# Performance work log

Measured on AMD Instinct MI355X. Metric: run time of the kernel, lower is better.

## Reference

```python
import jax, jax.numpy as jnp
import numpy as np

B, CIN, COUT, H, W, KK = 1, 32, 64, 181, 360, 4
NNZ_PER, NNZ_PER1 = 9, 4


def _make_psi(rng, K, H, W, nnz_per):
    # Sparse DISCO basis in COO form for longitude 0 (shift-invariant in lon).
    E = K * H * nnz_per
    seg = np.repeat(np.arange(K * H, dtype=np.int32), nnz_per)  # k*H + ho
    ho = seg % H
    dlat = rng.integers(-1, 2, size=E).astype(np.int32)
    hi = np.clip(ho + dlat, 0, H - 1).astype(np.int32)
    wi = (rng.integers(-1, 2, size=E).astype(np.int32)) % W
    vals = (rng.normal(size=E) * 0.2).astype(np.float32)
    return seg, hi, wi, vals


def setup_inputs() -> dict:
    rng = np.random.default_rng(0)
    key = jax.random.key(0)
    ks = jax.random.split(key, 5)
    x = jax.random.normal(ks[0], (B, CIN, H, W), dtype=jnp.float32)
    # spherical quadrature weights: sin(colatitude) * cell area
    theta = np.linspace(0.0, np.pi, H)
    qw = (np.sin(theta) * (np.pi / (H - 1)) * (2.0 * np.pi / W)).astype(np.float32)
    qw = np.maximum(qw, 1e-8).reshape(H, 1)
    seg, hi, wi, vals = _make_psi(rng, KK, H, W, NNZ_PER)
    seg1, hi1, wi1, vals1 = _make_psi(rng, 1, H, W, NNZ_PER1)
    w_depth = jax.random.normal(ks[1], (CIN, KK), dtype=jnp.float32) / np.sqrt(KK)
    w_point = jax.random.normal(ks[2], (COUT, CIN), dtype=jnp.float32) / np.sqrt(CIN)
    bias = jax.random.normal(ks[3], (COUT,), dtype=jnp.float32) * 0.02
    return {
        "x": x,
        "quad_w": jnp.asarray(qw),
        "vals": jnp.asarray(vals),
        "seg": jnp.asarray(seg),
        "hi": jnp.asarray(hi),
        "wi": jnp.asarray(wi),
        "w_depth": w_depth,
        "vals1": jnp.asarray(vals1),
        "seg1": jnp.asarray(seg1),
        "hi1": jnp.asarray(hi1),
        "wi1": jnp.asarray(wi1),
        "w_point": w_point,
        "bias": bias,
        "K": KK,
    }


def _disco_contract(x, vals, seg, hi, wi, K):
    # x: [B,C,H,W]; COO psi at lon 0; out[b,c,k,ho,wo] =
    #   sum_{e: seg[e]==k*H+ho} vals[e] * x[b,c,hi[e],(wi[e]+wo) mod W]
    Bq, C, Hq, Wq = x.shape
    rows = x[:, :, hi, :]                                        # [B,C,E,W]
    col = (wi[:, None] + jnp.arange(Wq, dtype=wi.dtype)[None, :]) % Wq  # [E,W]
    rolled = jnp.take_along_axis(rows, col[None, None, :, :], axis=3)   # [B,C,E,W]
    weighted = rolled * vals[None, None, :, None]
    out = jax.ops.segment_sum(weighted.transpose(2, 0, 1, 3), seg,
                              num_segments=K * Hq)               # [K*H,B,C,W]
    return out.reshape(K, Hq, Bq, C, Wq).transpose(2, 3, 0, 1, 4)  # [B,C,K,H,W]


def reference(x, quad_w, vals, seg, hi, wi, w_depth, vals1, seg1, hi1, wi1,
              w_point, bias, K):
    # depthwise DISCO conv (groups=C_in, no bias)
    xq = x * quad_w                                   # quadrature weighting
    xd = _disco_contract(xq, vals, seg, hi, wi, K)    # [B,C,K,H,W]
    y = jnp.einsum("ck,bckhw->bchw", w_depth, xd)     # per-channel K mix
    # pointwise DISCO conv (kernel_shape=1) = CLinear
    yq = y * quad_w
    z = _disco_contract(yq, vals1, seg1, hi1, wi1, 1)[:, :, 0]  # [B,C,H,W]
    out = jnp.einsum("oc,bchw->bohw", w_point, z) + bias[None, :, None, None]
    return out
```

## Files before the change

kernel.cpp:

```cpp
#include <hip/hip_runtime.h>


#define H_    181
#define W_    360
#define CIN_  32
#define COUT_ 64
#define K_    4
#define NNZ_  9
#define NNZ1_ 4
#define HW_   (H_*W_)
#define NT_   (NNZ1_*K_*NNZ_)

__global__ __launch_bounds__(512) void sepconv_one(
    const float* __restrict__ x, const float* __restrict__ quad_w,
    const float* __restrict__ vals, const int* __restrict__ hi,
    const int* __restrict__ wi, const float* __restrict__ w_depth,
    const float* __restrict__ vals1, const int* __restrict__ hi1,
    const int* __restrict__ wi1, const float* __restrict__ w_point,
    const float* __restrict__ bias, float* __restrict__ out)
{
    const int bx = blockIdx.x;
    const int h  = (bx & 7) * 23 + (bx >> 3);
    if (h >= H_) return;
    const int seg = blockIdx.y;
    const int w0  = seg * 64;
    const int pxn = (seg == 5) ? 40 : 64;
    const int gn  = pxn >> 2;
    const int tid = threadIdx.x;

    __shared__ float Tval[NT_];
    __shared__ int   Tbin[NT_];
    __shared__ float S[K_][25];
    __shared__ float C[CIN_][25];
    __shared__ float zs[64][33];

    const int g = tid & 15;
    const int c = tid >> 4;
    const bool act = (g < gn);

    int rowoff[5];
    #pragma unroll
    for (int rb = 0; rb < 5; ++rb) {
        int r = h - 2 + rb;
        r = (r < 0) ? 0 : ((r > H_ - 1) ? H_ - 1 : r);
        rowoff[rb] = r * W_;
    }

    const int bw = w0 + g * 4;
    const int cA = (bw + W_ - 4) % W_;
    const int cB = bw;
    const int cC = (bw + 4) % W_;

    float4 L[15];
    if (act) {
        const float* xc = x + c * HW_;
        #pragma unroll
        for (int rb = 0; rb < 5; ++rb) {
            const float* xr = xc + rowoff[rb];
            L[rb * 3 + 0] = *(const float4*)(xr + cA);
            L[rb * 3 + 1] = *(const float4*)(xr + cB);
            L[rb * 3 + 2] = *(const float4*)(xr + cC);
        }
    }

    if (tid < NT_) {
        const int a   = tid / 36;
        const int rem = tid - a * 36;
        const int k   = rem / 9;
        const int j   = rem - k * 9;
        const int e1  = h * NNZ1_ + a;
        const int m   = hi1[e1];
        const int w1  = wi1[e1];
        const int d1  = (w1 == 1) ? 1 : ((w1 == 0) ? 0 : -1);
        const int e   = (k * H_ + m) * NNZ_ + j;
        const int r   = hi[e];
        const int ww  = wi[e];
        const int d   = (ww == 1) ? 1 : ((ww == 0) ? 0 : -1);
        Tval[tid] = vals1[e1] * quad_w[m] * vals[e] * quad_w[r];
        Tbin[tid] = (r - h + 2) * 5 + (d1 + d + 2);
    }
    __syncthreads();

    if (tid < K_ * 25) {
        const int k   = tid / 25;
        const int bin = tid - k * 25;
        float s = 0.f;
        #pragma unroll
        for (int a = 0; a < NNZ1_; ++a)
            #pragma unroll
            for (int j = 0; j < NNZ_; ++j) {
                const int t2 = a * 36 + k * 9 + j;
                if (Tbin[t2] == bin) s += Tval[t2];
            }
        S[k][bin] = s;
    }
    __syncthreads();

    if (tid < CIN_ * 25) {
        const int cc = tid / 25, bin = tid - cc * 25;
        float acc = 0.f;
        #pragma unroll
        for (int k = 0; k < K_; ++k) acc += w_depth[cc * K_ + k] * S[k][bin];
        C[cc][bin] = acc;
    }
    if (tid + 512 < CIN_ * 25) {
        const int i2 = tid + 512;
        const int cc = i2 / 25, bin = i2 - cc * 25;
        float acc = 0.f;
        #pragma unroll
        for (int k = 0; k < K_; ++k) acc += w_depth[cc * K_ + k] * S[k][bin];
        C[cc][bin] = acc;
    }
    __syncthreads();

    if (act) {
        const float* Cc = &C[c][0];
        float a0 = 0.f, a1 = 0.f, a2 = 0.f, a3 = 0.f;
        #pragma unroll
        for (int rb = 0; rb < 5; ++rb) {
            const float4 vA = L[rb * 3 + 0];
            const float4 vB = L[rb * 3 + 1];
            const float4 vC = L[rb * 3 + 2];
            const float k0 = Cc[rb * 5 + 0], k1 = Cc[rb * 5 + 1],
                        k2 = Cc[rb * 5 + 2], k3 = Cc[rb * 5 + 3],
                        k4 = Cc[rb * 5 + 4];
            a0 += k0 * vA.z + k1 * vA.w + k2 * vB.x + k3 * vB.y + k4 * vB.z;
            a1 += k0 * vA.w + k1 * vB.x + k2 * vB.y + k3 * vB.z + k4 * vB.w;
            a2 += k0 * vB.x + k1 * vB.y + k2 * vB.z + k3 * vB.w + k4 * vC.x;
            a3 += k0 * vB.y + k1 * vB.z + k2 * vB.w + k3 * vC.x + k4 * vC.y;
        }
        const int p = g * 4;
        zs[p + 0][c] = a0;
        zs[p + 1][c] = a1;
        zs[p + 2][c] = a2;
        zs[p + 3][c] = a3;
    }
    __syncthreads();

    const int j  = tid & 63;
    const int oh = tid >> 6;
    if (j < pxn) {
        float zr[CIN_];
        #pragma unroll
        for (int cc = 0; cc < CIN_; ++cc) zr[cc] = zs[j][cc];

        const float* wp = w_point + oh * 8 * CIN_;
        float* op = out + oh * 8 * HW_ + h * W_ + w0 + j;
        #pragma unroll
        for (int oo = 0; oo < 8; ++oo) {
            float acc = bias[oh * 8 + oo];
            #pragma unroll
            for (int cc = 0; cc < CIN_; ++cc)
                acc += wp[oo * CIN_ + cc] * zr[cc];
            op[oo * HW_] = acc;
        }
    }
}

extern "C" void kernel_launch(void* const* d_in, const int* in_sizes, int n_in,
                              void* d_out, int out_size, void* d_ws, size_t ws_size,
                              hipStream_t stream) {
    const float* x       = (const float*)d_in[0];
    const float* quad_w  = (const float*)d_in[1];
    const float* vals    = (const float*)d_in[2];
    const int*   hi      = (const int*)d_in[4];
    const int*   wi      = (const int*)d_in[5];
    const float* w_depth = (const float*)d_in[6];
    const float* vals1   = (const float*)d_in[7];
    const int*   hi1     = (const int*)d_in[9];
    const int*   wi1     = (const int*)d_in[10];
    const float* w_point = (const float*)d_in[11];
    const float* bias    = (const float*)d_in[12];

    sepconv_one<<<dim3(184, 6), 512, 0, stream>>>(
        x, quad_w, vals, hi, wi, w_depth, vals1, hi1, wi1,
        w_point, bias, (float*)d_out);
}
```

Before: 115.5 us.

## Split per-row coefficient build into a separate prepass kernel

Moves construction of the fused per-latitude 5x5 stencil coefficients (sparse basis folding, quadrature weights, depthwise mix) out of the main kernel into a small prepass kernel that writes them to workspace once per row. Before, each of the six longitude segments rebuilt the same coefficients with three block barriers. The main kernel now loads them with float2 copies. The cost is an extra kernel launch and a global round trip for the coefficients.

```diff
diff --git a/kernel.cpp b/kernel.cpp
--- a/kernel.cpp
+++ b/kernel.cpp
@@ -10,58 +10,21 @@
 #define NNZ1_ 4
 #define HW_   (H_*W_)
 #define NT_   (NNZ1_*K_*NNZ_)
+#define CSZ_  (CIN_*25)
 
-__global__ __launch_bounds__(512) void sepconv_one(
-    const float* __restrict__ x, const float* __restrict__ quad_w,
-    const float* __restrict__ vals, const int* __restrict__ hi,
-    const int* __restrict__ wi, const float* __restrict__ w_depth,
-    const float* __restrict__ vals1, const int* __restrict__ hi1,
-    const int* __restrict__ wi1, const float* __restrict__ w_point,
-    const float* __restrict__ bias, float* __restrict__ out)
+__global__ __launch_bounds__(256) void coef_build(
+    const float* __restrict__ quad_w, const float* __restrict__ vals,
+    const int* __restrict__ hi, const int* __restrict__ wi,
+    const float* __restrict__ w_depth, const float* __restrict__ vals1,
+    const int* __restrict__ hi1, const int* __restrict__ wi1,
+    float* __restrict__ Cg)
 {
-    const int bx = blockIdx.x;
-    const int h  = (bx & 7) * 23 + (bx >> 3);
-    if (h >= H_) return;
-    const int seg = blockIdx.y;
-    const int w0  = seg * 64;
-    const int pxn = (seg == 5) ? 40 : 64;
-    const int gn  = pxn >> 2;
+    const int h   = blockIdx.x;
     const int tid = threadIdx.x;
 
     __shared__ float Tval[NT_];
     __shared__ int   Tbin[NT_];
     __shared__ float S[K_][25];
-    __shared__ float C[CIN_][25];
-    __shared__ float zs[64][33];
-
-    const int g = tid & 15;
-    const int c = tid >> 4;
-    const bool act = (g < gn);
-
-    int rowoff[5];
-    #pragma unroll
-    for (int rb = 0; rb < 5; ++rb) {
-        int r = h - 2 + rb;
-        r = (r < 0) ? 0 : ((r > H_ - 1) ? H_ - 1 : r);
-        rowoff[rb] = r * W_;
-    }
-
-    const int bw = w0 + g * 4;
-    const int cA = (bw + W_ - 4) % W_;
-    const int cB = bw;
-    const int cC = (bw + 4) % W_;
-
-    float4 L[15];
-    if (act) {
-        const float* xc = x + c * HW_;
-        #pragma unroll
-        for (int rb = 0; rb < 5; ++rb) {
-            const float* xr = xc + rowoff[rb];
-            L[rb * 3 + 0] = *(const float4*)(xr + cA);
-            L[rb * 3 + 1] = *(const float4*)(xr + cB);
-            L[rb * 3 + 2] = *(const float4*)(xr + cC);
-        }
-    }
 
     if (tid < NT_) {
         const int a   = tid / 36;
@@ -96,21 +59,64 @@
     }
     __syncthreads();
 
-    if (tid < CIN_ * 25) {
-        const int cc = tid / 25, bin = tid - cc * 25;
+    for (int i = tid; i < CSZ_; i += 256) {
+        const int cc = i / 25, bin = i - cc * 25;
         float acc = 0.f;
         #pragma unroll
         for (int k = 0; k < K_; ++k) acc += w_depth[cc * K_ + k] * S[k][bin];
-        C[cc][bin] = acc;
+        Cg[h * CSZ_ + i] = acc;
     }
-    if (tid + 512 < CIN_ * 25) {
-        const int i2 = tid + 512;
-        const int cc = i2 / 25, bin = i2 - cc * 25;
-        float acc = 0.f;
+}
+
+__global__ __launch_bounds__(512) void sepconv_main(
+    const float* __restrict__ x, const float* __restrict__ Cg,
+    const float* __restrict__ w_point, const float* __restrict__ bias,
+    float* __restrict__ out)
+{
+    const int bx = blockIdx.x;
+    const int h  = (bx & 7) * 23 + (bx >> 3);
+    if (h >= H_) return;
+    const int seg = blockIdx.y;
+    const int w0  = seg * 64;
+    const int pxn = (seg == 5) ? 40 : 64;
+    const int gn  = pxn >> 2;
+    const int tid = threadIdx.x;
+
+    __shared__ __attribute__((aligned(16))) float C[CIN_][25];
+    __shared__ float zs[64][33];
+
+    const int g = tid & 15;
+    const int c = tid >> 4;
+    const bool act = (g < gn);
+
+    int rowoff[5];
+    #pragma unroll
+    for (int rb = 0; rb < 5; ++rb) {
+        int r = h - 2 + rb;
+        r = (r < 0) ? 0 : ((r > H_ - 1) ? H_ - 1 : r);
+        rowoff[rb] = r * W_;
+    }
+
+    const int bw = w0 + g * 4;
+    const int cA = (bw + W_ - 4) % W_;
+    const int cB = bw;
+    const int cC = (bw + 4) % W_;
+
+    float4 L[15];
+    if (act) {
+        const float* xc = x + c * HW_;
         #pragma unroll
-        for (int k = 0; k < K_; ++k) acc += w_depth[cc * K_ + k] * S[k][bin];
-        C[cc][bin] = acc;
+        for (int rb = 0; rb < 5; ++rb) {
+            const float* xr = xc + rowoff[rb];
+            L[rb * 3 + 0] = *(const float4*)(xr + cA);
+            L[rb * 3 + 1] = *(const float4*)(xr + cB);
+            L[rb * 3 + 2] = *(const float4*)(xr + cC);
+        }
     }
+
+    if (tid < CSZ_ / 2)
+        ((float2*)&C[0][0])[tid] =
+            ((const float2*)(Cg + h * CSZ_))[tid];
     __syncthreads();
 
     if (act) {
@@ -172,7 +178,10 @@
     const float* w_point = (const float*)d_in[11];
     const float* bias    = (const float*)d_in[12];
 
-    sepconv_one<<<dim3(184, 6), 512, 0, stream>>>(
-        x, quad_w, vals, hi, wi, w_depth, vals1, hi1, wi1,
-        w_point, bias, (float*)d_out);
+    float* Cg = (float*)d_ws;
+
+    coef_build<<<dim3(181), 256, 0, stream>>>(
+        quad_w, vals, hi, wi, w_depth, vals1, hi1, wi1, Cg);
+    sepconv_main<<<dim3(184, 6), 512, 0, stream>>>(
+        x, Cg, w_point, bias, (float*)d_out);
 }
```

Result: no change. 115.9 us (+0.4%).
